# Performance work log

Measured on AMD Instinct MI355X. Metric: run time of the kernel, lower is better.

Reference implementation:

```python
import jax, jax.numpy as jnp
import numpy as np

B, S, HID, NH = 1, 2048, 2048, 16
HD = HID // NH
HALF = HD // 2
# quantization scales (registered buffers / pack() scales in the original module)
ATTN_IN_SCALE = 0.02   # attn_input_scale: dequant scale of int8 hidden_states
Q_OUT_SCALE = 0.05     # q_output_scale
K_OUT_SCALE = 0.05     # k_output_scale
V_OUT_SCALE = 0.04     # v_output_scale
Q_ROT_SCALE = 0.06     # q_rotary_output_scale
K_ROT_SCALE = 0.06     # k_rotary_output_scale
OUT_IN_SCALE = 0.03    # out_input_scale
W_ALPHA = 0.002        # folded int8 GEMM alpha for q/k/v W8A8B8O8Linear
BETA = 1.0             # bias scale of W8A8B8O8Linear
O_ALPHA = 0.001        # folded alpha for o_proj W8A8BFP32OFP32Linear
PROB_SCALE = 1.0 / 127.0  # attention-prob int8 quant scale
INV_SQRT_HD = float(1.0 / np.sqrt(HD))


def _q8(x):
    # saturating int8 quantization (values kept in float32)
    return jnp.clip(jnp.round(x), -127.0, 127.0)


def setup_inputs() -> dict:
    key = jax.random.key(0)
    ks = jax.random.split(key, 10)
    hidden_states = jax.random.normal(ks[0], (B, S, HID), jnp.float32)
    pos = jnp.arange(S, dtype=jnp.float32)
    inv_freq = 1.0 / (10000.0 ** (jnp.arange(0, HD, 2, dtype=jnp.float32) / HD))
    freqs = pos[:, None] * inv_freq[None, :]          # (S, HD//2)
    cos, sin = jnp.cos(freqs), jnp.sin(freqs)
    w8 = lambda k: jax.random.randint(k, (HID, HID), -127, 128).astype(jnp.float32)
    b8 = lambda k: jax.random.randint(k, (HID,), -127, 128).astype(jnp.float32)
    return dict(
        hidden_states=hidden_states, cos=cos, sin=sin,
        wq=w8(ks[1]), wk=w8(ks[2]), wv=w8(ks[3]), wo=w8(ks[4]),
        bq=b8(ks[5]), bk=b8(ks[6]), bv=b8(ks[7]),
        bo=jax.random.normal(ks[8], (HID,), jnp.float32) * 0.01,
    )


def reference(hidden_states, cos, sin, wq, wk, wv, wo, bq, bk, bv, bo):
    # quantize activations to int8 (done upstream of the module in smoothquant)
    x8 = _q8(hidden_states / ATTN_IN_SCALE)                       # (B,S,HID) int8 vals

    # W8A8B8O8Linear: int8 GEMM, alpha-scaled, int8 bias, saturate to int8
    def lin8(x, w, b):
        return _q8(jnp.einsum('bsi,oi->bso', x, w) * W_ALPHA + BETA * b)

    q8, k8, v8 = lin8(x8, wq, bq), lin8(x8, wk, bk), lin8(x8, wv, bv)

    # int8_rotary_embedding_fwd: dequant -> split-half rotary -> requant
    def rope(x8_flat, in_scale, out_scale):
        x = x8_flat.reshape(B, S, NH, HD) * in_scale
        x0, x1 = x[..., :HALF], x[..., HALF:]
        c, s_ = cos[None, :, None, :], sin[None, :, None, :]
        rot = jnp.concatenate([x0 * c - x1 * s_, x0 * s_ + x1 * c], axis=-1)
        return _q8(rot / out_scale)

    q = rope(q8, Q_OUT_SCALE, Q_ROT_SCALE)                        # (B,S,NH,HD)
    k = rope(k8, K_OUT_SCALE, K_ROT_SCALE)
    v = v8.reshape(B, S, NH, HD)

    # smooth_llama_context_attn_fwd: int8 QK^T -> fp32 scores -> causal softmax
    scores = jnp.einsum('bqhd,bkhd->bhqk', q, k) * (Q_ROT_SCALE * K_ROT_SCALE * INV_SQRT_HD)
    causal = jnp.tril(jnp.ones((S, S), bool))
    scores = jnp.where(causal[None, None], scores, -1e9)
    p = jax.nn.softmax(scores, axis=-1)
    p8 = _q8(p * 127.0)                                           # quantize probs to int8
    # int8 PV bmm, rescale and saturate to int8 for o_proj input
    o8 = _q8(jnp.einsum('bhqk,bkhd->bqhd', p8, v) * (PROB_SCALE * V_OUT_SCALE / OUT_IN_SCALE))
    o8 = o8.reshape(B, S, HID)

    # W8A8BFP32OFP32Linear: int8 GEMM, fp32 alpha + fp32 bias
    out = jnp.einsum('bso,po->bsp', o8, wo) * O_ALPHA + bo
    return out
```

## Files before the change

kernel.cpp:

```cpp
#include <hip/hip_runtime.h>
#include <math.h>

typedef __attribute__((ext_vector_type(4))) int i32x4;
typedef signed char s8;

constexpr int S   = 2048;
constexpr int HID = 2048;
constexpr int NH  = 16;
constexpr int HD  = 128;
constexpr int HALF = 64;

#define SCORE_SCALE ((float)(0.06 * 0.06 * 0.08838834764831845))
#define OSCALE      ((float)(((1.0 / 127.0) * 0.04) / 0.03))

__device__ __forceinline__ float clip127(float r){
  return fminf(fmaxf(r, -127.0f), 127.0f);
}
__device__ __forceinline__ i32x4 mfma_i8(i32x4 a, i32x4 b, i32x4 c){
  return __builtin_amdgcn_mfma_i32_16x16x64_i8(a, b, c, 0, 0, 0);
}
__device__ __forceinline__ void async16(const void* g, void* l){
  __builtin_amdgcn_global_load_lds(
      (const __attribute__((address_space(1))) unsigned*)g,
      (__attribute__((address_space(3))) unsigned*)l, 16, 0, 0);
}
template<int ROWS>
__device__ __forceinline__ void stage_async_swz(s8* dst, const s8* src, int stride){
  const int tid = threadIdx.x;
#pragma unroll
  for (int i = 0; i < ROWS/32; ++i){
    int o = i*256 + tid;
    int row = o >> 3, ch = o & 7;
    async16(src + (size_t)row*stride + ((ch ^ (row & 7))*16), dst + o*16);
  }
}
__device__ __forceinline__ i32x4 rd16(const s8* buf, int row, int ch){
  return *(const i32x4*)(buf + row*128 + ((ch ^ (row & 7))*16));
}
__device__ __forceinline__ void stage64(s8* dst, const s8* src, int stride){
  const int tid = threadIdx.x;
#pragma unroll
  for (int i = 0; i < 2; ++i){
    int o = i*256 + tid;
    int row = o >> 2, slot = o & 3;
    int ch = slot ^ ((row >> 2) & 3);
    async16(src + (size_t)row*stride + ch*16, dst + o*16);
  }
}
__device__ __forceinline__ i32x4 rd64(const s8* buf, int row, int g){
  return *(const i32x4*)(buf + row*64 + ((g ^ ((row >> 2) & 3))*16));
}
__device__ __forceinline__ int tri_qt(int t){
  int qt = (int)((sqrtf(8.f*t + 1.f) - 1.f)*0.5f);
  while ((qt+1)*(qt+2)/2 <= t) ++qt;
  while (qt*(qt+1)/2 > t) --qt;
  return qt;
}

__global__ void cvt_all(const float* __restrict__ hid, const float* __restrict__ wq,
                        const float* __restrict__ wk, const float* __restrict__ wv,
                        const float* __restrict__ wo, s8* __restrict__ xd,
                        s8* __restrict__ qd, s8* __restrict__ kd,
                        s8* __restrict__ vd, s8* __restrict__ od, int n){
  const float* srcs[5] = {hid, wq, wk, wv, wo};
  s8* dsts[5] = {xd, qd, kd, vd, od};
  int which = blockIdx.y;
  const float* src = srcs[which];
  s8* dst = dsts[which];
  int i = (blockIdx.x * blockDim.x + threadIdx.x) * 4;
  if (i >= n) return;
  float4 v = *(const float4*)(src + i);
  float x[4] = {v.x, v.y, v.z, v.w};
  unsigned packed = 0;
#pragma unroll
  for (int j = 0; j < 4; ++j){
    int b;
    if (which == 0) b = (int)clip127(rintf(x[j] / 0.02f));
    else            b = (int)x[j];
    packed |= ((unsigned)(b & 255)) << (8*j);
  }
  *(unsigned*)(dst + i) = packed;
}

__global__ __launch_bounds__(256)
void gemm_qkv(const s8* __restrict__ A, const s8* __restrict__ W,
              const float* __restrict__ bq, const float* __restrict__ bk,
              const float* __restrict__ bv, s8* __restrict__ Out){
#pragma clang fp contract(off)
  constexpr int Kd = 2048, N = 2048, NT = 32;
  const int z = blockIdx.z;
  const s8* Bt = W + (size_t)z*(4u<<20);
  s8* Y = Out + (size_t)z*(4u<<20);
  const float* bss[3] = {bq, bk, bv};
  const float* bias = bss[z];
  __shared__ __attribute__((aligned(16))) s8 As[3][128*64];
  __shared__ __attribute__((aligned(16))) s8 Bs[3][128*64];
  const int lin = blockIdx.x + (blockIdx.y << 4);
  const int virt = (lin & 7)*32 + (lin >> 3);
  const int bm = virt & 15, bn = virt >> 4;
  const int tid = threadIdx.x;
  const int wid = tid >> 6, lane = tid & 63;
  const int wm = wid >> 1, wn = wid & 1;
  const int col16 = lane & 15, g = lane >> 4;
  i32x4 acc[4][4] = {};
  const s8* Ab = A + (size_t)(bm*128)*Kd;
  const s8* Bb = Bt + (size_t)(bn*128)*Kd;

  stage64(As[0], Ab, Kd);       stage64(Bs[0], Bb, Kd);
  stage64(As[1], Ab + 64, Kd);  stage64(Bs[1], Bb + 64, Kd);
  asm volatile("s_waitcnt vmcnt(4)" ::: "memory");
  __builtin_amdgcn_s_barrier();

  for (int T = 0; T < NT; ++T){
    const int nxt = T + 2;
    if (nxt < NT){
      stage64(As[nxt%3], Ab + nxt*64, Kd);
      stage64(Bs[nxt%3], Bb + nxt*64, Kd);
    }
    const s8* as = As[T%3];
    const s8* bs = Bs[T%3];
    i32x4 af[4], bf[4];
#pragma unroll
    for (int i = 0; i < 4; ++i) af[i] = rd64(as, wm*64 + i*16 + col16, g);
#pragma unroll
    for (int j = 0; j < 4; ++j) bf[j] = rd64(bs, wn*64 + j*16 + col16, g);
#pragma unroll
    for (int i = 0; i < 4; ++i)
#pragma unroll
      for (int j = 0; j < 4; ++j)
        acc[i][j] = mfma_i8(af[i], bf[j], acc[i][j]);
    if (nxt < NT) asm volatile("s_waitcnt vmcnt(4)" ::: "memory");
    else          asm volatile("s_waitcnt vmcnt(0)" ::: "memory");
    __builtin_amdgcn_s_barrier();
  }

#pragma unroll
  for (int i = 0; i < 4; ++i){
#pragma unroll
    for (int j = 0; j < 4; ++j){
      int row0 = bm*128 + wm*64 + i*16 + g*4;
      int col  = bn*128 + wn*64 + j*16 + col16;
#pragma unroll
      for (int r = 0; r < 4; ++r){
        float t = (float)acc[i][j][r] * 0.002f;
        t = t + bias[col];
        Y[(size_t)(row0 + r)*N + col] = (s8)(int)clip127(rintf(t));
      }
    }
  }
}

__global__ __launch_bounds__(256)
void gemm_o(const s8* __restrict__ A, const s8* __restrict__ Bt,
            const float* __restrict__ bias, float* __restrict__ Y){
#pragma clang fp contract(off)
  constexpr int Kd = 2048, N = 2048;
  __shared__ __attribute__((aligned(16))) s8 As[128*128];
  __shared__ __attribute__((aligned(16))) s8 Bs[64*128];
  const int lin = blockIdx.x + (blockIdx.y << 4);
  const int virt = (lin & 7)*64 + (lin >> 3);
  const int bm = virt & 15, bn = virt >> 4;
  const int tid = threadIdx.x;
  const int wid = tid >> 6, lane = tid & 63;
  const int wm = wid >> 1, wn = wid & 1;
  const int col16 = lane & 15, g = lane >> 4;
  i32x4 acc[4][2] = {};
  const s8* Ab = A + (size_t)(bm*128)*Kd;
  const s8* Bb = Bt + (size_t)(bn*64)*Kd;
  for (int kt = 0; kt < 16; ++kt){
    stage_async_swz<128>(As, Ab + kt*128, Kd);
    stage_async_swz<64>(Bs, Bb + kt*128, Kd);
    __syncthreads();
#pragma unroll
    for (int kk = 0; kk < 2; ++kk){
      i32x4 af[4], bf[2];
#pragma unroll
      for (int i = 0; i < 4; ++i) af[i] = rd16(As, wm*64 + i*16 + col16, kk*4 + g);
#pragma unroll
      for (int j = 0; j < 2; ++j) bf[j] = rd16(Bs, wn*32 + j*16 + col16, kk*4 + g);
#pragma unroll
      for (int i = 0; i < 4; ++i)
#pragma unroll
        for (int j = 0; j < 2; ++j)
          acc[i][j] = mfma_i8(af[i], bf[j], acc[i][j]);
    }
    __syncthreads();
  }
#pragma unroll
  for (int i = 0; i < 4; ++i){
#pragma unroll
    for (int j = 0; j < 2; ++j){
      int row0 = bm*128 + wm*64 + i*16 + g*4;
      int col  = bn*64 + wn*32 + j*16 + col16;
#pragma unroll
      for (int r = 0; r < 4; ++r){
        float t = (float)acc[i][j][r] * 0.001f;
        t = t + bias[col];
        Y[(size_t)(row0 + r)*N + col] = t;
      }
    }
  }
}

__global__ void rope_qk(s8* __restrict__ q, s8* __restrict__ k,
                        const float* __restrict__ cosp, const float* __restrict__ sinp){
#pragma clang fp contract(off)
  int idx = blockIdx.x * blockDim.x + threadIdx.x;
  int t4 = (idx & 15) * 4;
  int h  = (idx >> 4) & (NH-1);
  int s  = idx >> 8;
  if (s >= S) return;
  float4 c4 = *(const float4*)(cosp + s*HALF + t4);
  float4 s4 = *(const float4*)(sinp + s*HALF + t4);
  float cc[4] = {c4.x, c4.y, c4.z, c4.w}, ss[4] = {s4.x, s4.y, s4.z, s4.w};
  int base = s*HID + h*HD + t4;
  {
    int a0 = *(const int*)(q + base), a1 = *(const int*)(q + base + HALF);
    unsigned o0 = 0, o1 = 0;
#pragma unroll
    for (int j = 0; j < 4; ++j){
      float x0 = (float)((s8)(a0 >> (8*j))) * 0.05f;
      float x1 = (float)((s8)(a1 >> (8*j))) * 0.05f;
      float r0 = x0*cc[j] - x1*ss[j];
      float r1 = x0*ss[j] + x1*cc[j];
      o0 |= ((unsigned)(((int)clip127(rintf(r0 / 0.06f))) & 255)) << (8*j);
      o1 |= ((unsigned)(((int)clip127(rintf(r1 / 0.06f))) & 255)) << (8*j);
    }
    *(unsigned*)(q + base) = o0; *(unsigned*)(q + base + HALF) = o1;
  }
  {
    int a0 = *(const int*)(k + base), a1 = *(const int*)(k + base + HALF);
    unsigned o0 = 0, o1 = 0;
#pragma unroll
    for (int j = 0; j < 4; ++j){
      float x0 = (float)((s8)(a0 >> (8*j))) * 0.05f;
      float x1 = (float)((s8)(a1 >> (8*j))) * 0.05f;
      float r0 = x0*cc[j] - x1*ss[j];
      float r1 = x0*ss[j] + x1*cc[j];
      o0 |= ((unsigned)(((int)clip127(rintf(r0 / 0.06f))) & 255)) << (8*j);
      o1 |= ((unsigned)(((int)clip127(rintf(r1 / 0.06f))) & 255)) << (8*j);
    }
    *(unsigned*)(k + base) = o0; *(unsigned*)(k + base + HALF) = o1;
  }
}

__global__ void vtrans(const s8* __restrict__ v, s8* __restrict__ vt){
  __shared__ __attribute__((aligned(16))) s8 t[128*144];
  int s0 = blockIdx.x * 128, h = blockIdx.y;
  int tid = threadIdx.x;
#pragma unroll
  for (int i = 0; i < 4; ++i){
    int vv = i*256 + tid, r = vv >> 3, ch = vv & 7;
    *(i32x4*)(t + r*144 + ch*16) = *(const i32x4*)(v + (size_t)(s0 + r)*HID + h*HD + ch*16);
  }
  __syncthreads();
#pragma unroll
  for (int i = 0; i < 4; ++i){
    int vv = i*256 + tid, d = vv >> 3, sc = (vv & 7)*16;
    s8 tmp[16];
#pragma unroll
    for (int j = 0; j < 16; ++j) tmp[j] = t[(sc + j)*144 + d];
    *(i32x4*)(vt + (size_t)(h*HD + d)*S + s0 + sc) = *(i32x4*)tmp;
  }
}

__global__ __launch_bounds__(256)
void attn_stats(const s8* __restrict__ qr, const s8* __restrict__ kr,
                float2* __restrict__ stats){
  const int x = blockIdx.x, h = blockIdx.y;
  const int tri = x >> 1, half = x & 1;
  const int qt = tri_qt(tri);
  const int kt = tri - qt*(qt+1)/2;
  const int q0 = qt*128 + half*64;
  const int tid = threadIdx.x, wid = tid >> 6, lane = tid & 63;
  const int col16 = lane & 15, g = lane >> 4;
  __shared__ __attribute__((aligned(16))) s8 Ks[128*128];

  stage_async_swz<128>(Ks, kr + (size_t)(kt*128)*HID + h*HD, HID);
  const s8* qb = qr + (size_t)(q0 + wid*16 + col16)*HID + h*HD + g*16;
  i32x4 aq[2];
  aq[0] = *(const i32x4*)(qb);
  aq[1] = *(const i32x4*)(qb + 64);
  __syncthreads();

  i32x4 sc[8] = {};
#pragma unroll
  for (int kk = 0; kk < 2; ++kk){
#pragma unroll
    for (int j = 0; j < 8; ++j){
      i32x4 bk = rd16(Ks, j*16 + col16, kk*4 + g);
      sc[j] = mfma_i8(aq[kk], bk, sc[j]);
    }
  }

  const bool diag = (kt == qt);
#pragma unroll
  for (int r = 0; r < 4; ++r){
    int rit = half*64 + wid*16 + g*4 + r;
    int qrow = qt*128 + rit;
    int mi = (int)0x80000000;
#pragma unroll
    for (int j = 0; j < 8; ++j){
      int v = sc[j][r];
      if (diag && (kt*128 + j*16 + col16 > qrow)) v = (int)0x80000000;
      mi = max(mi, v);
    }
    mi = max(mi, __shfl_xor(mi, 1));
    mi = max(mi, __shfl_xor(mi, 2));
    mi = max(mi, __shfl_xor(mi, 4));
    mi = max(mi, __shfl_xor(mi, 8));
    float mf = (float)mi * SCORE_SCALE;
    float st = 0.f;
#pragma unroll
    for (int j = 0; j < 8; ++j){
      float arg;
      if (diag && (kt*128 + j*16 + col16 > qrow)) arg = -1e30f;
      else arg = (float)sc[j][r] * SCORE_SCALE - mf;
      st += __expf(arg);
    }
    st += __shfl_xor(st, 1);
    st += __shfl_xor(st, 2);
    st += __shfl_xor(st, 4);
    st += __shfl_xor(st, 8);
    if (col16 == 0) stats[(size_t)(h*136 + tri)*128 + rit] = make_float2(mf, st);
  }
}

__global__ void attn_reduce(const float2* __restrict__ stats, float2* __restrict__ ml){
  const int row = threadIdx.x, qt = blockIdx.x, h = blockIdx.y;
  const int tri = qt*(qt+1)/2;
  float m = -3.0e38f;
  for (int kt = 0; kt <= qt; ++kt)
    m = fmaxf(m, stats[(size_t)(h*136 + tri + kt)*128 + row].x);
  float l = 0.f;
  for (int kt = 0; kt <= qt; ++kt){
    float2 s = stats[(size_t)(h*136 + tri + kt)*128 + row];
    l += s.y * __expf(s.x - m);
  }
  ml[(h*16 + qt)*128 + row] = make_float2(m, l);
}

__global__ __launch_bounds__(256)
void attn_score(const s8* __restrict__ qr, const s8* __restrict__ kr,
                const float2* __restrict__ ml, s8* __restrict__ P8){
  const int x = blockIdx.x, h = blockIdx.y;
  const int tri = x >> 1, half = x & 1;
  const int qt = tri_qt(tri);
  const int kt = tri - qt*(qt+1)/2;
  const int q0 = qt*128 + half*64;
  const int tid = threadIdx.x, wid = tid >> 6, lane = tid & 63;
  const int col16 = lane & 15, g = lane >> 4;
  __shared__ __attribute__((aligned(16))) s8 Ks[128*128];
  __shared__ __attribute__((aligned(16))) s8 Pl[64*128];

  stage_async_swz<128>(Ks, kr + (size_t)(kt*128)*HID + h*HD, HID);
  const s8* qb = qr + (size_t)(q0 + wid*16 + col16)*HID + h*HD + g*16;
  i32x4 aq[2];
  aq[0] = *(const i32x4*)(qb);
  aq[1] = *(const i32x4*)(qb + 64);
  float m[4], c[4];
#pragma unroll
  for (int r = 0; r < 4; ++r){
    float2 t = ml[(h*16 + qt)*128 + half*64 + wid*16 + g*4 + r];
    m[r] = t.x;
    c[r] = 127.0f / t.y;
  }
  __syncthreads();

  const bool diag = (kt == qt);
#pragma unroll
  for (int j = 0; j < 8; ++j){
    i32x4 s0 = {};
    s0 = mfma_i8(aq[0], rd16(Ks, j*16 + col16, g), s0);
    s0 = mfma_i8(aq[1], rd16(Ks, j*16 + col16, 4 + g), s0);
    int colk = j*16 + col16;
#pragma unroll
    for (int r = 0; r < 4; ++r){
      int row = wid*16 + g*4 + r;
      int qrow = q0 + row;
      float p8v = 0.0f;
      if (!diag || (kt*128 + colk) <= qrow){
        float sv = (float)s0[r] * SCORE_SCALE;
        p8v = clip127(rintf(__expf(sv - m[r]) * c[r]));
      }
      Pl[row*128 + colk] = (s8)(int)p8v;
    }
  }
  __syncthreads();
  s8* dst = P8 + (size_t)(h*136 + tri)*16384 + half*8192;
#pragma unroll
  for (int i = 0; i < 2; ++i){
    int o = i*256 + tid;
    *(i32x4*)(dst + o*16) = *(const i32x4*)(Pl + o*16);
  }
}

__global__ __launch_bounds__(256)
void attn_pv(const s8* __restrict__ P8, const s8* __restrict__ vt8,
             s8* __restrict__ o8){
  const int qt = 15 - blockIdx.x;
  const int h = blockIdx.y, dh = blockIdx.z;
  const int tri = qt*(qt+1)/2;
  const int tid = threadIdx.x, wid = tid >> 6, lane = tid & 63;
  const int wm = wid >> 1, wn = wid & 1;
  const int col16 = lane & 15, g = lane >> 4;
  __shared__ __attribute__((aligned(16))) s8 Ps[128*128];
  __shared__ __attribute__((aligned(16))) s8 Vs[64*128];

  i32x4 acc[4][2] = {};
  for (int kt = 0; kt <= qt; ++kt){
    stage_async_swz<128>(Ps, P8 + (size_t)(h*136 + tri + kt)*16384, 128);
    stage_async_swz<64>(Vs, vt8 + (size_t)(h*HD + dh*64)*S + kt*128, S);
    __syncthreads();
#pragma unroll
    for (int kk = 0; kk < 2; ++kk){
      i32x4 af[4], bf[2];
#pragma unroll
      for (int i = 0; i < 4; ++i) af[i] = rd16(Ps, wm*64 + i*16 + col16, kk*4 + g);
#pragma unroll
      for (int j = 0; j < 2; ++j) bf[j] = rd16(Vs, wn*32 + j*16 + col16, kk*4 + g);
#pragma unroll
      for (int i = 0; i < 4; ++i)
#pragma unroll
        for (int j = 0; j < 2; ++j)
          acc[i][j] = mfma_i8(af[i], bf[j], acc[i][j]);
    }
    __syncthreads();
  }
#pragma unroll
  for (int i = 0; i < 4; ++i)
#pragma unroll
    for (int j = 0; j < 2; ++j)
#pragma unroll
      for (int r = 0; r < 4; ++r){
        int row = qt*128 + wm*64 + i*16 + g*4 + r;
        int d = dh*64 + wn*32 + j*16 + col16;
        o8[(size_t)row*HID + h*HD + d] = (s8)(int)clip127(rintf((float)acc[i][j][r] * OSCALE));
      }
}

extern "C" void kernel_launch(void* const* d_in, const int* in_sizes, int n_in,
                              void* d_out, int out_size, void* d_ws, size_t ws_size,
                              hipStream_t stream) {
  const float* hidden = (const float*)d_in[0];
  const float* cosp   = (const float*)d_in[1];
  const float* sinp   = (const float*)d_in[2];
  const float* wq     = (const float*)d_in[3];
  const float* wk     = (const float*)d_in[4];
  const float* wv     = (const float*)d_in[5];
  const float* wo     = (const float*)d_in[6];
  const float* bq     = (const float*)d_in[7];
  const float* bk     = (const float*)d_in[8];
  const float* bv     = (const float*)d_in[9];
  const float* bo     = (const float*)d_in[10];
  float* out = (float*)d_out;

  const size_t MB = 1024*1024;
  s8* ws8 = (s8*)d_ws;
  s8* x8  = ws8 + 0*MB;
  s8* wq8 = ws8 + 4*MB;
  s8* wk8 = ws8 + 8*MB;
  s8* wv8 = ws8 + 12*MB;
  s8* wo8 = ws8 + 16*MB;
  s8* q8  = ws8 + 20*MB;
  s8* k8  = ws8 + 24*MB;
  s8* v8  = ws8 + 28*MB;
  s8* vt8 = ws8 + 32*MB;
  s8* P8  = ws8 + 36*MB;
  s8* o8  = x8;
  float2* stats = (float2*)(ws8 + 4*MB);
  float2* mlb   = (float2*)(ws8 + 4*MB + 2400*1024);

  const int n = HID*HID;
  dim3 b256(256);

  cvt_all<<<dim3(n/1024, 5), b256, 0, stream>>>(hidden, wq, wk, wv, wo,
                                                x8, wq8, wk8, wv8, wo8, n);

  gemm_qkv<<<dim3(16, 16, 3), b256, 0, stream>>>(x8, wq8, bq, bk, bv, q8);

  rope_qk<<<(S*NH*16)/256, b256, 0, stream>>>(q8, k8, cosp, sinp);
  vtrans<<<dim3(S/128, NH), b256, 0, stream>>>(v8, vt8);

  attn_stats<<<dim3(272, 16), b256, 0, stream>>>(q8, k8, stats);
  attn_reduce<<<dim3(16, 16), dim3(128), 0, stream>>>(stats, mlb);
  attn_score<<<dim3(272, 16), b256, 0, stream>>>(q8, k8, mlb, P8);
  attn_pv<<<dim3(16, 16, 2), b256, 0, stream>>>(P8, vt8, o8);

  gemm_o<<<dim3(16, 32), b256, 0, stream>>>(o8, wo8, bo, out);
}
```

Baseline: 144.4 us.

## Triple-buffer async LDS staging in o_proj GEMM and attention PV kernels

Moves gemm_o and attn_pv from a load-then-sync single-buffer loop to a three-stage ring of LDS buffers. Two tiles are prefetched ahead with async global-to-LDS loads, and partial vmcnt waits replace full __syncthreads. gemm_o also switches to 64-wide K tiles using the rd64 swizzle. stage64 is templated on row count so it can serve both tile shapes. The aim is to hide global load latency behind MFMA work. In exchange, attn_pv needs three times the LDS (72KB), which may reduce occupancy, and the hand-counted vmcnt values must match the exact number of loads issued.

New measurement: 147.2 us. No clear change (+2.0%).

```diff
diff --git a/kernel.cpp b/kernel.cpp
--- a/kernel.cpp
+++ b/kernel.cpp
@@ -37,10 +37,11 @@
 __device__ __forceinline__ i32x4 rd16(const s8* buf, int row, int ch){
   return *(const i32x4*)(buf + row*128 + ((ch ^ (row & 7))*16));
 }
+template<int ROWS>
 __device__ __forceinline__ void stage64(s8* dst, const s8* src, int stride){
   const int tid = threadIdx.x;
 #pragma unroll
-  for (int i = 0; i < 2; ++i){
+  for (int i = 0; i < ROWS/64; ++i){
     int o = i*256 + tid;
     int row = o >> 2, slot = o & 3;
     int ch = slot ^ ((row >> 2) & 3);
@@ -106,16 +107,16 @@
   const s8* Ab = A + (size_t)(bm*128)*Kd;
   const s8* Bb = Bt + (size_t)(bn*128)*Kd;
 
-  stage64(As[0], Ab, Kd);       stage64(Bs[0], Bb, Kd);
-  stage64(As[1], Ab + 64, Kd);  stage64(Bs[1], Bb + 64, Kd);
+  stage64<128>(As[0], Ab, Kd);       stage64<128>(Bs[0], Bb, Kd);
+  stage64<128>(As[1], Ab + 64, Kd);  stage64<128>(Bs[1], Bb + 64, Kd);
   asm volatile("s_waitcnt vmcnt(4)" ::: "memory");
   __builtin_amdgcn_s_barrier();
 
   for (int T = 0; T < NT; ++T){
     const int nxt = T + 2;
     if (nxt < NT){
-      stage64(As[nxt%3], Ab + nxt*64, Kd);
-      stage64(Bs[nxt%3], Bb + nxt*64, Kd);
+      stage64<128>(As[nxt%3], Ab + nxt*64, Kd);
+      stage64<128>(Bs[nxt%3], Bb + nxt*64, Kd);
     }
     const s8* as = As[T%3];
     const s8* bs = Bs[T%3];
@@ -154,9 +155,9 @@
 void gemm_o(const s8* __restrict__ A, const s8* __restrict__ Bt,
             const float* __restrict__ bias, float* __restrict__ Y){
 #pragma clang fp contract(off)
-  constexpr int Kd = 2048, N = 2048;
-  __shared__ __attribute__((aligned(16))) s8 As[128*128];
-  __shared__ __attribute__((aligned(16))) s8 Bs[64*128];
+  constexpr int Kd = 2048, N = 2048, NT = 32;
+  __shared__ __attribute__((aligned(16))) s8 As[3][128*64];
+  __shared__ __attribute__((aligned(16))) s8 Bs[3][64*64];
   const int lin = blockIdx.x + (blockIdx.y << 4);
   const int virt = (lin & 7)*64 + (lin >> 3);
   const int bm = virt & 15, bn = virt >> 4;
@@ -167,25 +168,35 @@
   i32x4 acc[4][2] = {};
   const s8* Ab = A + (size_t)(bm*128)*Kd;
   const s8* Bb = Bt + (size_t)(bn*64)*Kd;
-  for (int kt = 0; kt < 16; ++kt){
-    stage_async_swz<128>(As, Ab + kt*128, Kd);
-    stage_async_swz<64>(Bs, Bb + kt*128, Kd);
-    __syncthreads();
-#pragma unroll
-    for (int kk = 0; kk < 2; ++kk){
-      i32x4 af[4], bf[2];
-#pragma unroll
-      for (int i = 0; i < 4; ++i) af[i] = rd16(As, wm*64 + i*16 + col16, kk*4 + g);
-#pragma unroll
-      for (int j = 0; j < 2; ++j) bf[j] = rd16(Bs, wn*32 + j*16 + col16, kk*4 + g);
-#pragma unroll
-      for (int i = 0; i < 4; ++i)
-#pragma unroll
-        for (int j = 0; j < 2; ++j)
-          acc[i][j] = mfma_i8(af[i], bf[j], acc[i][j]);
-    }
-    __syncthreads();
-  }
+
+  stage64<128>(As[0], Ab, Kd);       stage64<64>(Bs[0], Bb, Kd);
+  stage64<128>(As[1], Ab + 64, Kd);  stage64<64>(Bs[1], Bb + 64, Kd);
+  asm volatile("s_waitcnt vmcnt(3)" ::: "memory");
+  __builtin_amdgcn_s_barrier();
+
+  for (int T = 0; T < NT; ++T){
+    const int nxt = T + 2;
+    if (nxt < NT){
+      stage64<128>(As[nxt%3], Ab + nxt*64, Kd);
+      stage64<64>(Bs[nxt%3], Bb + nxt*64, Kd);
+    }
+    const s8* as = As[T%3];
+    const s8* bs = Bs[T%3];
+    i32x4 af[4], bf[2];
+#pragma unroll
+    for (int i = 0; i < 4; ++i) af[i] = rd64(as, wm*64 + i*16 + col16, g);
+#pragma unroll
+    for (int j = 0; j < 2; ++j) bf[j] = rd64(bs, wn*32 + j*16 + col16, g);
+#pragma unroll
+    for (int i = 0; i < 4; ++i)
+#pragma unroll
+      for (int j = 0; j < 2; ++j)
+        acc[i][j] = mfma_i8(af[i], bf[j], acc[i][j]);
+    if (nxt < NT) asm volatile("s_waitcnt vmcnt(3)" ::: "memory");
+    else          asm volatile("s_waitcnt vmcnt(0)" ::: "memory");
+    __builtin_amdgcn_s_barrier();
+  }
+
 #pragma unroll
   for (int i = 0; i < 4; ++i){
 #pragma unroll
@@ -401,32 +412,49 @@
   const int qt = 15 - blockIdx.x;
   const int h = blockIdx.y, dh = blockIdx.z;
   const int tri = qt*(qt+1)/2;
+  const int nt = qt + 1;
   const int tid = threadIdx.x, wid = tid >> 6, lane = tid & 63;
   const int wm = wid >> 1, wn = wid & 1;
   const int col16 = lane & 15, g = lane >> 4;
-  __shared__ __attribute__((aligned(16))) s8 Ps[128*128];
-  __shared__ __attribute__((aligned(16))) s8 Vs[64*128];
+  __shared__ __attribute__((aligned(16))) s8 Ps[3][128*128];
+  __shared__ __attribute__((aligned(16))) s8 Vs[3][64*128];
+
+#define PV_STAGE(t) do{ \
+    stage_async_swz<128>(Ps[(t)%3], P8 + (size_t)(h*136 + tri + (t))*16384, 128); \
+    stage_async_swz<64>(Vs[(t)%3], vt8 + (size_t)(h*HD + dh*64)*S + (t)*128, S); \
+  }while(0)
 
   i32x4 acc[4][2] = {};
-  for (int kt = 0; kt <= qt; ++kt){
-    stage_async_swz<128>(Ps, P8 + (size_t)(h*136 + tri + kt)*16384, 128);
-    stage_async_swz<64>(Vs, vt8 + (size_t)(h*HD + dh*64)*S + kt*128, S);
-    __syncthreads();
+  PV_STAGE(0);
+  if (nt > 1) PV_STAGE(1);
+  if (nt > 1) asm volatile("s_waitcnt vmcnt(6)" ::: "memory");
+  else        asm volatile("s_waitcnt vmcnt(0)" ::: "memory");
+  __builtin_amdgcn_s_barrier();
+
+  for (int T = 0; T < nt; ++T){
+    const int nxt = T + 2;
+    if (nxt < nt) PV_STAGE(nxt);
+    const s8* ps = Ps[T%3];
+    const s8* vs = Vs[T%3];
 #pragma unroll
     for (int kk = 0; kk < 2; ++kk){
       i32x4 af[4], bf[2];
 #pragma unroll
-      for (int i = 0; i < 4; ++i) af[i] = rd16(Ps, wm*64 + i*16 + col16, kk*4 + g);
-#pragma unroll
-      for (int j = 0; j < 2; ++j) bf[j] = rd16(Vs, wn*32 + j*16 + col16, kk*4 + g);
+      for (int i = 0; i < 4; ++i) af[i] = rd16(ps, wm*64 + i*16 + col16, kk*4 + g);
+#pragma unroll
+      for (int j = 0; j < 2; ++j) bf[j] = rd16(vs, wn*32 + j*16 + col16, kk*4 + g);
 #pragma unroll
       for (int i = 0; i < 4; ++i)
 #pragma unroll
         for (int j = 0; j < 2; ++j)
           acc[i][j] = mfma_i8(af[i], bf[j], acc[i][j]);
     }
-    __syncthreads();
-  }
+    if (nxt < nt) asm volatile("s_waitcnt vmcnt(6)" ::: "memory");
+    else          asm volatile("s_waitcnt vmcnt(0)" ::: "memory");
+    __builtin_amdgcn_s_barrier();
+  }
+#undef PV_STAGE
+
 #pragma unroll
   for (int i = 0; i < 4; ++i)
 #pragma unroll
```
